# Performance work log

Hardware: AMD Instinct MI355X
Metric: run time of the kernel (lower is better)

The kernel has to match this reference:

```python
import jax, jax.numpy as jnp
import numpy as np
from jax import lax

L, B, S, D, H = 4, 4, 2048, 1024, 2048
EPS = 1e-5


def setup_inputs() -> dict:
    key = jax.random.key(0)
    ks = jax.random.split(key, 8)

    def rn(k, shape, fan_in, fan_out):
        scale = (2.0 / (fan_in + fan_out)) ** 0.5  # xavier-ish
        return jax.random.normal(k, shape, jnp.float32) * scale

    return {
        "x": jax.random.normal(ks[0], (B, S, D), jnp.float32),
        "Wp1": rn(ks[1], (L, H, D), D, H),
        "bp1": jnp.zeros((L, H), jnp.float32),
        "Wp2": rn(ks[2], (L, H, D), D, H),
        "bp2": jnp.zeros((L, H), jnp.float32),
        "convW": rn(ks[3], (L, H, H, 3), 3 * H, H),  # torch Conv1d layout (O, I, K)
        "convb": jnp.zeros((L, H), jnp.float32),
        "Wz": rn(ks[4], (L, H, H), H, H),
        "bz": jnp.zeros((L, H), jnp.float32),
        "Wh": rn(ks[5], (L, H, H), H, H),
        "bh": jnp.zeros((L, H), jnp.float32),
        "Wd": rn(ks[6], (L, D, H), H, D),
        "bd": jnp.zeros((L, D), jnp.float32),
        # 4 LayerNorms per layer: [strand1_ln1, conv_ln, gru_ln, strand2_ln1]
        "ln_g": jnp.ones((L, 4, H), jnp.float32),
        "ln_b": jnp.zeros((L, 4, H), jnp.float32),
    }


def _ln(x, g, b):
    m = jnp.mean(x, axis=-1, keepdims=True)
    xc = x - m
    v = jnp.mean(xc * xc, axis=-1, keepdims=True)
    return xc * lax.rsqrt(v + EPS) * g + b


def _log_g(x):
    return jnp.where(x >= 0, jnp.log(jax.nn.relu(x) + 0.5), -jax.nn.softplus(-x))


def _min_gru(x, Wz, bz, Wh, bh):
    # x: (B, S, H); training-mode log-space parallel scan, h_0 = 0
    k = jnp.einsum('bsh,oh->bso', x, Wz) + bz
    log_z = -jax.nn.softplus(-k)
    log_coeffs = -jax.nn.softplus(k)
    log_h0 = jnp.full((x.shape[0], 1, Wz.shape[0]), jnp.log(0.5), x.dtype)  # log_g(0)
    log_tilde_h = _log_g(jnp.einsum('bsh,oh->bso', x, Wh) + bh)
    log_values = jnp.concatenate([log_h0, log_z + log_tilde_h], axis=1)  # (B,S+1,H)
    a_star = jnp.pad(jnp.cumsum(log_coeffs, axis=1), ((0, 0), (1, 0), (0, 0)))
    log_h = a_star + lax.cumlogsumexp(log_values - a_star, axis=1)
    return jnp.exp(log_h)[:, 1:]


def _conv1d(x, w, b):
    # x: (B, S, H) -> NCH conv with kernel 3, same padding
    y = lax.conv_general_dilated(
        x.transpose(0, 2, 1), w, window_strides=(1,), padding=((1, 1),),
        dimension_numbers=('NCH', 'OIH', 'NCH'))
    return (y + b[None, :, None]).transpose(0, 2, 1)


def _forward(x, Wp1, bp1, Wp2, bp2, convW, convb, Wz, bz, Wh, bh, Wd, bd, ln_g, ln_b):
    for i in range(L):
        s1 = _ln(jnp.einsum('bsd,hd->bsh', x, Wp1[i]) + bp1[i], ln_g[i, 0], ln_b[i, 0])
        s1 = _ln(_conv1d(s1, convW[i], convb[i]), ln_g[i, 1], ln_b[i, 1])
        s1 = jax.nn.silu(s1)
        s1 = _min_gru(s1, Wz[i], bz[i], Wh[i], bh[i])
        s1 = _ln(s1, ln_g[i, 2], ln_b[i, 2])
        s2 = jax.nn.silu(_ln(jnp.einsum('bsd,hd->bsh', x, Wp2[i]) + bp2[i], ln_g[i, 3], ln_b[i, 3]))
        x = jnp.einsum('bsh,dh->bsd', s1 * s2, Wd[i]) + bd[i] + x
    return x


def reference(x, Wp1, bp1, Wp2, bp2, convW, convb, Wz, bz, Wh, bh, Wd, bd, ln_g, ln_b):
    return _forward(x, Wp1, bp1, Wp2, bp2, convW, convb, Wz, bz, Wh, bh, Wd, bd, ln_g, ln_b)
```

## Files before the change

### kernel.cpp

```cpp
#include <hip/hip_runtime.h>

typedef unsigned short u16;
typedef short  s16x8 __attribute__((ext_vector_type(8)));
typedef float  f32x4 __attribute__((ext_vector_type(4)));
typedef unsigned short u16x4 __attribute__((ext_vector_type(4)));

#define LDS_AS __attribute__((address_space(3)))
#define GLB_AS __attribute__((address_space(1)))

__device__ __forceinline__ float bf2f(u16 x) {
    unsigned u = ((unsigned)x) << 16;
    return __builtin_bit_cast(float, u);
}
__device__ __forceinline__ u16 f2bf(float f) {
    unsigned u = __builtin_bit_cast(unsigned, f);
    return (u16)((u + 0x7FFFu + ((u >> 16) & 1u)) >> 16);
}
__device__ __forceinline__ void gload16(const u16* g, u16* l) {
    __builtin_amdgcn_global_load_lds((const GLB_AS unsigned int*)g,
                                     (LDS_AS unsigned int*)l, 16, 0, 0);
}

static constexpr int Lc = 4, Sc = 2048, Dc = 1024, Hc = 2048, Mc = 8192;
static constexpr int CH = 64, CL = 32;
static constexpr int NCHAN = 4 * Hc;
static constexpr int KPW = 4096;

#define BAR() __builtin_amdgcn_s_barrier()
#define VMCNT(n) asm volatile("s_waitcnt vmcnt(" #n ")" ::: "memory")

#define READ_A(d, BUF, MH)                                                     \
    _Pragma("unroll") for (int mf = 0; mf < 4; ++mf) {                         \
        d[mf][0] = *(const s16x8*)(aB0 + (BUF)*16384 + (MH)*4096 + mf*1024);   \
        d[mf][1] = *(const s16x8*)(aB1 + (BUF)*16384 + (MH)*4096 + mf*1024);   \
    }
#define READ_B(BUF, NH)                                                        \
    _Pragma("unroll") for (int jb = 0; jb < 2; ++jb) {                         \
        bq[jb][0] = *(const s16x8*)(bB0 + (BUF)*16384 + (NH)*2048 + jb*1024);  \
        bq[jb][1] = *(const s16x8*)(bB1 + (BUF)*16384 + (NH)*2048 + jb*1024);  \
    }
#define QUAD(a, MH, NH)                                                        \
    _Pragma("unroll") for (int mf = 0; mf < 4; ++mf)                           \
    _Pragma("unroll") for (int jb = 0; jb < 2; ++jb)                           \
    _Pragma("unroll") for (int kk = 0; kk < 2; ++kk)                           \
        acc[(MH)*4 + mf][(NH)*2 + jb] = __builtin_amdgcn_mfma_f32_16x16x32_bf16( \
            a[mf][kk], bq[jb][kk], acc[(MH)*4 + mf][(NH)*2 + jb], 0, 0, 0);

#define STAGE_A(BUF, H, KT) {                                                  \
    if (CONV) {                                                                \
        const int seg_ = ((KT)*64) >> 11;                                      \
        const int kb_  = ((KT)*64) & (Hc - 1);                                 \
        const int r0_  = convRow + (H)*128 + seg_;                             \
        const u16* s0_ = ((unsigned)(r0_ - bb) < (unsigned)Sc)                 \
                             ? A + (size_t)r0_ * lda + kb_ + scol : zerobuf;   \
        const u16* s1_ = ((unsigned)(r0_ + 8 - bb) < (unsigned)Sc)             \
                             ? A + (size_t)(r0_ + 8) * lda + kb_ + scol : zerobuf; \
        gload16(s0_, ldsA + (BUF)*16384 + (H)*8192);                           \
        gload16(s1_, ldsA + (BUF)*16384 + (H)*8192 + 512);                     \
    } else {                                                                   \
        const u16* s_ = srcA + (size_t)((H)*128) * lda + (KT)*64;              \
        gload16(s_,                   ldsA + (BUF)*16384 + (H)*8192);          \
        gload16(s_ + 8*(size_t)lda,   ldsA + (BUF)*16384 + (H)*8192 + 512);    \
    } }
#define STAGE_B(BUF, H, KT) {                                                  \
    const u16* s_ = srcB + (size_t)((H)*128) * K + (KT)*64;                    \
    gload16(s_,                 ldsB + (BUF)*16384 + (H)*8192);                \
    gload16(s_ + 8*(size_t)K,   ldsB + (BUF)*16384 + (H)*8192 + 512);          \
}

template <int CONV, int REPS>
__global__ __launch_bounds__(512, 2)
void gemm8(const u16* __restrict__ A, const u16* __restrict__ Bw,
           const float* __restrict__ bias, u16* __restrict__ Cb,
           int M, int N, int K, int lda, const u16* __restrict__ zerobuf) {
    (void)M;
    __shared__ __align__(16) u16 As[2][256][64];
    __shared__ __align__(16) u16 Bs[2][256][64];

    const int tid = threadIdx.x;
    const int w = tid >> 6, l = tid & 63;
    const int wm = w & 1, wn = w >> 1;

    const unsigned nwg = gridDim.x * gridDim.y;
    unsigned id = blockIdx.x + gridDim.x * blockIdx.y;
    id = (id & 7u) * (nwg >> 3) + (id >> 3);
    const int bx = (int)(id % gridDim.x);
    const int byBase = (int)(id / gridDim.x);
    const int colBase = bx * 256;

    const int srow = w * 16 + (l >> 3);
    const int scol = ((l & 7) ^ (l >> 3)) << 3;
    const u16* srcB = Bw + (size_t)(colBase + srow) * K + scol;
    u16* const ldsA = &As[0][0][0] + w * 1024;
    u16* const ldsB = &Bs[0][0][0] + w * 1024;

    const int r16 = l & 15, slot = l >> 4;
    const int swz = (r16 & 7) << 4;
    const int co0 = (((slot << 4)      ) ^ swz) >> 1;
    const int co1 = (((slot << 4) | 64 ) ^ swz) >> 1;
    const u16* aB0 = &As[0][0][0] + (wm * 128 + r16) * 64 + co0;
    const u16* aB1 = &As[0][0][0] + (wm * 128 + r16) * 64 + co1;
    const u16* bB0 = &Bs[0][0][0] + (wn * 64  + r16) * 64 + co0;
    const u16* bB1 = &Bs[0][0][0] + (wn * 64  + r16) * 64 + co1;

    const int coll = colBase + wn * 64 + r16;

    for (int rep = 0; rep < REPS; ++rep) {
        const int rowBase = (byBase + rep * gridDim.y) * 256;
        const u16* srcA = A + (size_t)(rowBase + srow) * lda + scol;
        const int bb = rowBase & ~(Sc - 1);
        const int convRow = rowBase + srow - 1;

        f32x4 acc[8][4];
#pragma unroll
        for (int m = 0; m < 8; ++m)
#pragma unroll
            for (int n = 0; n < 4; ++n)
#pragma unroll
                for (int r = 0; r < 4; ++r) acc[m][n][r] = 0.f;

        s16x8 a0[4][2], a1[4][2], bq[2][2];

        STAGE_A(0, 0, 0); STAGE_A(0, 1, 0); STAGE_B(0, 0, 0); STAGE_B(0, 1, 0);
        VMCNT(4);
        STAGE_A(1, 0, 1); STAGE_A(1, 1, 1); STAGE_B(1, 0, 1);
        VMCNT(6);
        BAR();

        const int NI = K >> 7;
        for (int i = 0; i < NI; ++i) {
            const int t1 = 2 * i + 1, t2 = 2 * i + 2, t3 = 2 * i + 3;
            const bool more = (i + 1 < NI);
            READ_A(a0, 0, 0); READ_B(0, 0);
            STAGE_B(1, 1, t1);
            BAR();
            __builtin_amdgcn_s_setprio(1); QUAD(a0, 0, 0); __builtin_amdgcn_s_setprio(0);
            BAR();
            READ_A(a1, 0, 1);
            BAR();
            __builtin_amdgcn_s_setprio(1); QUAD(a1, 1, 0); __builtin_amdgcn_s_setprio(0);
            BAR();
            READ_B(0, 1);
            if (more) { STAGE_A(0, 0, t2); STAGE_A(0, 1, t2); }
            BAR();
            __builtin_amdgcn_s_setprio(1); QUAD(a0, 0, 1); __builtin_amdgcn_s_setprio(0);
            BAR();
            if (more) STAGE_B(0, 0, t2);
            BAR();
            __builtin_amdgcn_s_setprio(1); QUAD(a1, 1, 1); __builtin_amdgcn_s_setprio(0);
            if (more) { VMCNT(6); } else { VMCNT(0); }
            BAR();
            READ_A(a0, 1, 0); READ_B(1, 0);
            if (more) STAGE_B(0, 1, t2);
            BAR();
            __builtin_amdgcn_s_setprio(1); QUAD(a0, 0, 0); __builtin_amdgcn_s_setprio(0);
            BAR();
            READ_A(a1, 1, 1);
            BAR();
            __builtin_amdgcn_s_setprio(1); QUAD(a1, 1, 0); __builtin_amdgcn_s_setprio(0);
            BAR();
            READ_B(1, 1);
            if (more) { STAGE_A(1, 0, t3); STAGE_A(1, 1, t3); }
            BAR();
            __builtin_amdgcn_s_setprio(1); QUAD(a0, 0, 1); __builtin_amdgcn_s_setprio(0);
            BAR();
            if (more) STAGE_B(1, 0, t3);
            BAR();
            __builtin_amdgcn_s_setprio(1); QUAD(a1, 1, 1); __builtin_amdgcn_s_setprio(0);
            if (more) VMCNT(6);
            BAR();
        }

        const int row00 = rowBase + wm * 128 + slot * 4;
#pragma unroll
        for (int m8 = 0; m8 < 8; ++m8) {
#pragma unroll
            for (int n4 = 0; n4 < 4; ++n4) {
                const int col = coll + n4 * 16;
                const float bv = bias[col];
                const int row0 = row00 + m8 * 16;
#pragma unroll
                for (int r = 0; r < 4; ++r)
                    Cb[(size_t)(row0 + r) * N + col] = f2bf(acc[m8][n4][r] + bv);
            }
        }
    }
}

template <int CONV, int EPI>
__global__ __launch_bounds__(256)
void gemm_bt(const u16* __restrict__ A, const u16* __restrict__ Bw,
             const float* __restrict__ bias,
             u16* __restrict__ Cb, float* __restrict__ Cf,
             const float* __restrict__ resid, u16* __restrict__ xout,
             int M, int N, int K, int lda, const u16* __restrict__ zerobuf) {
    __shared__ __align__(16) u16 As[128 * 32];
    __shared__ __align__(16) u16 Bs[128 * 32];
    const int tid  = threadIdx.x;
    const int wave = tid >> 6, lane = tid & 63;
    const int rowBase = blockIdx.y * 128;
    const int colBase = blockIdx.x * 128;
    const int srow = tid >> 2;
    const int scol = (tid & 3) << 3;

    u16* ldsA0 = As + wave * 512;
    u16* ldsA1 = As + 2048 + wave * 512;
    u16* ldsB0 = Bs + wave * 512;
    u16* ldsB1 = Bs + 2048 + wave * 512;

    const u16* bpt0 = Bw + (size_t)(colBase + srow) * K + scol;
    const u16* bpt1 = Bw + (size_t)(colBase + 64 + srow) * K + scol;
    const int arow0 = rowBase + srow;
    const int arow1 = arow0 + 64;
    const u16* ap0 = A + (size_t)arow0 * lda + scol;
    const u16* ap1 = A + (size_t)arow1 * lda + scol;

    const int wm = wave & 1, wn = wave >> 1;
    const int mB = wm * 64, nB = wn * 64;
    const int quad = lane >> 4, l16 = lane & 15;

    f32x4 acc[4][4];
#pragma unroll
    for (int a = 0; a < 4; a++)
#pragma unroll
        for (int b = 0; b < 4; b++)
#pragma unroll
            for (int r = 0; r < 4; r++) acc[a][b][r] = 0.f;

    for (int k0 = 0; k0 < K; k0 += 32) {
        if (CONV) {
            const int seg = k0 >> 11;
            const int kk  = (k0 & (Hc - 1)) + scol;
            const int bbb = rowBase & ~(Sc - 1);
            const int r0  = arow0 + seg - 1;
            const int r1  = arow1 + seg - 1;
            const u16* g0 = ((unsigned)(r0 - bbb) < (unsigned)Sc) ? A + (size_t)r0 * lda + kk : zerobuf;
            const u16* g1 = ((unsigned)(r1 - bbb) < (unsigned)Sc) ? A + (size_t)r1 * lda + kk : zerobuf;
            gload16(g0, ldsA0);
            gload16(g1, ldsA1);
        } else {
            gload16(ap0 + k0, ldsA0);
            gload16(ap1 + k0, ldsA1);
        }
        gload16(bpt0 + k0, ldsB0);
        gload16(bpt1 + k0, ldsB1);
        __syncthreads();

        s16x8 af[4], bfr[4];
#pragma unroll
        for (int t = 0; t < 4; t++)
            af[t] = *(const s16x8*)(As + (mB + t * 16 + l16) * 32 + (quad << 3));
#pragma unroll
        for (int t = 0; t < 4; t++)
            bfr[t] = *(const s16x8*)(Bs + (nB + t * 16 + l16) * 32 + (quad << 3));
#pragma unroll
        for (int mt = 0; mt < 4; mt++)
#pragma unroll
            for (int nt = 0; nt < 4; nt++)
                acc[mt][nt] = __builtin_amdgcn_mfma_f32_16x16x32_bf16(af[mt], bfr[nt], acc[mt][nt], 0, 0, 0);
        __syncthreads();
    }

#pragma unroll
    for (int mt = 0; mt < 4; mt++) {
#pragma unroll
        for (int nt = 0; nt < 4; nt++) {
            const int col  = colBase + nB + nt * 16 + l16;
            const int row0 = rowBase + mB + mt * 16 + (quad << 2);
            const float bv = bias[col];
#pragma unroll
            for (int r = 0; r < 4; r++) {
                const size_t idx = (size_t)(row0 + r) * N + col;
                float v = acc[mt][nt][r] + bv;
                if (EPI == 0) {
                    Cb[idx] = f2bf(v);
                } else {
                    v += resid[idx];
                    Cf[idx]   = v;
                    xout[idx] = f2bf(v);
                }
            }
        }
    }
}

__global__ __launch_bounds__(256)
void ln_fuse(const u16* __restrict__ in, int instride, u16* __restrict__ out,
             const float* __restrict__ g, const float* __restrict__ b,
             const u16* __restrict__ mul, int do_silu) {
    __shared__ float sred[4], qred[4];
    const int row = blockIdx.x, tid = threadIdx.x;
    const int lane = tid & 63, wave = tid >> 6;
    const size_t ibase = (size_t)row * instride + tid * 8;
    const size_t obase = (size_t)row * Hc + tid * 8;

    s16x8 v8 = *(const s16x8*)(in + ibase);
    float x[8];
#pragma unroll
    for (int j = 0; j < 8; j++) x[j] = bf2f((u16)v8[j]);
    float s = 0.f, q = 0.f;
#pragma unroll
    for (int j = 0; j < 8; j++) { s += x[j]; q += x[j] * x[j]; }
#pragma unroll
    for (int off = 32; off > 0; off >>= 1) {
        s += __shfl_down(s, off);
        q += __shfl_down(q, off);
    }
    if (lane == 0) { sred[wave] = s; qred[wave] = q; }
    __syncthreads();
    const float St = sred[0] + sred[1] + sred[2] + sred[3];
    const float Qt = qred[0] + qred[1] + qred[2] + qred[3];
    const float mean = St * (1.0f / Hc);
    const float var  = Qt * (1.0f / Hc) - mean * mean;
    const float rs   = rsqrtf(var + 1e-5f);

    const int c = tid * 8;
    const float4 g0 = *(const float4*)(g + c), g1 = *(const float4*)(g + c + 4);
    const float4 b0 = *(const float4*)(b + c), b1 = *(const float4*)(b + c + 4);
    const float gg[8] = {g0.x, g0.y, g0.z, g0.w, g1.x, g1.y, g1.z, g1.w};
    const float bb[8] = {b0.x, b0.y, b0.z, b0.w, b1.x, b1.y, b1.z, b1.w};
    s16x8 m8;
    if (mul) m8 = *(const s16x8*)(mul + obase);
    s16x8 o8;
#pragma unroll
    for (int j = 0; j < 8; j++) {
        float y = (x[j] - mean) * rs * gg[j] + bb[j];
        if (do_silu) y = y / (1.0f + __expf(-y));
        if (mul) y *= bf2f((u16)m8[j]);
        o8[j] = (short)f2bf(y);
    }
    *(s16x8*)(out + obase) = o8;
}

__device__ __forceinline__ void scan_step(float k, float p, float& ct, float& vt) {
    const float l1p = __logf(1.f + __expf(-fabsf(k)));
    ct = -(fmaxf(k, 0.f) + l1p);
    const float lg = (p >= 0.f) ? __logf(p + 0.5f)
                                : -(fmaxf(-p, 0.f) + __logf(1.f + __expf(-fabsf(p))));
    vt = -(fmaxf(-k, 0.f) + l1p) + lg;
}
__device__ __forceinline__ float laddexp(float a, float b) {
    const float m = fmaxf(a, b);
    return m + __logf(1.f + __expf(-fabsf(a - b)));
}

__global__ __launch_bounds__(256)
void scan_part1(const u16* __restrict__ kp,
                float* __restrict__ Cc, float* __restrict__ Vv) {
    const int tid = threadIdx.x;
    const int hb = blockIdx.x & 7;
    const int c  = (blockIdx.x >> 3) & 63;
    const int b  = blockIdx.x >> 9;
    const int h  = hb * 256 + tid;
    size_t idx = (size_t)(b * Sc + c * CL) * KPW + h;
    float C = 0.f, V = -1e30f;
#pragma unroll 4
    for (int t = 0; t < CL; t++) {
        float ct, vt;
        scan_step(bf2f(kp[idx]), bf2f(kp[idx + Hc]), ct, vt);
        V = laddexp(V + ct, vt);
        C += ct;
        idx += KPW;
    }
    const int chan = b * Hc + h;
    Cc[c * NCHAN + chan] = C;
    Vv[c * NCHAN + chan] = V;
}

__global__ __launch_bounds__(256)
void scan_mid(const float* __restrict__ Cc, const float* __restrict__ Vv,
              float* __restrict__ carry) {
    const int chan = blockIdx.x * 256 + threadIdx.x;
    float lh = -0.69314718f;
    for (int cb = 0; cb < CH; cb += 8) {
        float Cr[8], Vr[8];
#pragma unroll
        for (int j = 0; j < 8; j++) {
            Cr[j] = Cc[(cb + j) * NCHAN + chan];
            Vr[j] = Vv[(cb + j) * NCHAN + chan];
        }
#pragma unroll
        for (int j = 0; j < 8; j++) {
            carry[(cb + j) * NCHAN + chan] = lh;
            lh = laddexp(lh + Cr[j], Vr[j]);
        }
    }
}

__global__ __launch_bounds__(256)
void scan_part3(const u16* __restrict__ kp,
                const float* __restrict__ carry, u16* __restrict__ out) {
    const int tid = threadIdx.x;
    const int hb = blockIdx.x & 7;
    const int c  = (blockIdx.x >> 3) & 63;
    const int b  = blockIdx.x >> 9;
    const int h  = hb * 256 + tid;
    size_t idx = (size_t)(b * Sc + c * CL) * KPW + h;
    size_t odx = (size_t)(b * Sc + c * CL) * Hc + h;
    float lh = carry[c * NCHAN + (b * Hc + h)];
#pragma unroll 4
    for (int t = 0; t < CL; t++) {
        float ct, vt;
        scan_step(bf2f(kp[idx]), bf2f(kp[idx + Hc]), ct, vt);
        lh = laddexp(lh + ct, vt);
        out[odx] = f2bf(__expf(lh));
        idx += KPW;
        odx += Hc;
    }
}

__global__ __launch_bounds__(256)
void castf2b(const float* __restrict__ in, u16* __restrict__ out, int n) {
    const int i = (blockIdx.x * 256 + threadIdx.x) << 2;
    if (i >= n) return;
    const float4 v = *(const float4*)(in + i);
    u16x4 o;
    o.x = f2bf(v.x); o.y = f2bf(v.y); o.z = f2bf(v.z); o.w = f2bf(v.w);
    *(u16x4*)(out + i) = o;
}

__global__ __launch_bounds__(256)
void prep2(const float* __restrict__ srcA, const float* __restrict__ srcB,
           const float* __restrict__ bA, const float* __restrict__ bB,
           u16* __restrict__ dst, float* __restrict__ bias_dst, int nPerHalf) {
    const int bid = blockIdx.x, tid = threadIdx.x;
    const int halfBlocks = gridDim.x >> 1;
    const int half = (bid >= halfBlocks) ? 1 : 0;
    const size_t i = ((size_t)(bid - half * halfBlocks) * 256 + tid) * 4;
    const float* src = half ? srcB : srcA;
    const float4 v = *(const float4*)(src + i);
    u16x4 o;
    o.x = f2bf(v.x); o.y = f2bf(v.y); o.z = f2bf(v.z); o.w = f2bf(v.w);
    *(u16x4*)(dst + (size_t)half * nPerHalf + i) = o;
    if (bid < 4) {
        const int j = bid * 1024 + tid * 4;
        const float4 vb = (j < 2048) ? *(const float4*)(bA + j)
                                     : *(const float4*)(bB + (j - 2048));
        *(float4*)(bias_dst + j) = vb;
    }
}

__global__ __launch_bounds__(256)
void conv_tr(const float* __restrict__ w, u16* __restrict__ out) {
    const int idx = blockIdx.x * 256 + threadIdx.x;
    const float* src = w + (size_t)idx * 3;
    const float a = src[0], b = src[1], c = src[2];
    const int o = idx >> 11, ii = idx & (Hc - 1);
    u16* dst = out + (size_t)o * (3 * Hc) + ii;
    dst[0]        = f2bf(a);
    dst[Hc]       = f2bf(b);
    dst[2 * Hc]   = f2bf(c);
}

extern "C" void kernel_launch(void* const* d_in, const int* in_sizes, int n_in,
                              void* d_out, int out_size, void* d_ws, size_t ws_size,
                              hipStream_t stream) {
    (void)in_sizes; (void)n_in; (void)out_size;
    const float* x0    = (const float*)d_in[0];
    const float* Wp1   = (const float*)d_in[1];
    const float* bp1   = (const float*)d_in[2];
    const float* Wp2   = (const float*)d_in[3];
    const float* bp2   = (const float*)d_in[4];
    const float* convW = (const float*)d_in[5];
    const float* convb = (const float*)d_in[6];
    const float* Wz    = (const float*)d_in[7];
    const float* bz    = (const float*)d_in[8];
    const float* Wh    = (const float*)d_in[9];
    const float* bh    = (const float*)d_in[10];
    const float* Wd    = (const float*)d_in[11];
    const float* bd    = (const float*)d_in[12];
    const float* lng   = (const float*)d_in[13];
    const float* lnb   = (const float*)d_in[14];
    float* out = (float*)d_out;

    char* ws = (char*)d_ws;
    u16* wbuf = (u16*)(ws);
    u16* s1   = (u16*)(ws + 25165824);
    u16* t1   = (u16*)(ws + 58720256);
    u16* kp   = (u16*)(ws + 92274688);
    u16* s2   = kp;
    u16* xb   = (u16*)(ws + 159383552);
    u16* zero = (u16*)(ws + 176160768);
    float* scanC = (float*)(ws + 176161792);
    float* scanV = (float*)(ws + 178258944);
    float* carry = (float*)(ws + 180356096);
    float* bias2 = (float*)(ws + 182453248);
    u16* P       = (u16*)(ws + 184549376);
    const bool FUSEP = ws_size >= 251658240ull;

    hipMemsetAsync(zero, 0, 1024, stream);
    castf2b<<<dim3((Mc * Dc / 4) / 256), dim3(256), 0, stream>>>(x0, xb, Mc * Dc);

    const size_t wpStride = (size_t)Hc * Dc;
    const size_t cvStride = (size_t)Hc * Hc * 3;
    const size_t wzStride = (size_t)Hc * Hc;
    const size_t wdStride = (size_t)Dc * Hc;

    for (int i = 0; i < Lc; ++i) {
        const float* g0 = lng + ((size_t)i * 4 + 0) * Hc; const float* be0 = lnb + ((size_t)i * 4 + 0) * Hc;
        const float* g1 = lng + ((size_t)i * 4 + 1) * Hc; const float* be1 = lnb + ((size_t)i * 4 + 1) * Hc;
        const float* g2 = lng + ((size_t)i * 4 + 2) * Hc; const float* be2 = lnb + ((size_t)i * 4 + 2) * Hc;
        const float* g3 = lng + ((size_t)i * 4 + 3) * Hc; const float* be3 = lnb + ((size_t)i * 4 + 3) * Hc;

        if (FUSEP) {
            prep2<<<dim3(2 * (int)(wpStride / 1024)), dim3(256), 0, stream>>>(
                Wp1 + i * wpStride, Wp2 + i * wpStride,
                bp1 + (size_t)i * Hc, bp2 + (size_t)i * Hc, wbuf, bias2, (int)wpStride);
            gemm8<0, 2><<<dim3(KPW / 256, Mc / 512), dim3(512), 0, stream>>>(
                xb, wbuf, bias2, P, Mc, KPW, Dc, Dc, zero);
            ln_fuse<<<dim3(Mc), dim3(256), 0, stream>>>(P, KPW, s1, g0, be0, nullptr, 0);
        } else {
            castf2b<<<dim3((int)(wpStride / 4 / 256)), dim3(256), 0, stream>>>(Wp1 + i * wpStride, wbuf, (int)wpStride);
            gemm8<0, 2><<<dim3(Hc / 256, Mc / 512), dim3(512), 0, stream>>>(
                xb, wbuf, bp1 + (size_t)i * Hc, t1, Mc, Hc, Dc, Dc, zero);
            ln_fuse<<<dim3(Mc), dim3(256), 0, stream>>>(t1, Hc, s1, g0, be0, nullptr, 0);
        }

        conv_tr<<<dim3((Hc * Hc) / 256), dim3(256), 0, stream>>>(convW + i * cvStride, wbuf);
        gemm8<1, 1><<<dim3(Hc / 256, Mc / 256), dim3(512), 0, stream>>>(
            s1, wbuf, convb + (size_t)i * Hc, t1, Mc, Hc, 3 * Hc, Hc, zero);
        ln_fuse<<<dim3(Mc), dim3(256), 0, stream>>>(t1, Hc, s1, g1, be1, nullptr, 1);

        prep2<<<dim3(2 * (int)(wzStride / 1024)), dim3(256), 0, stream>>>(
            Wz + i * wzStride, Wh + i * wzStride,
            bz + (size_t)i * Hc, bh + (size_t)i * Hc, wbuf, bias2, (int)wzStride);
        gemm8<0, 2><<<dim3(KPW / 256, Mc / 512), dim3(512), 0, stream>>>(
            s1, wbuf, bias2, kp, Mc, KPW, Hc, Hc, zero);
        scan_part1<<<dim3(2048), dim3(256), 0, stream>>>(kp, scanC, scanV);
        scan_mid<<<dim3(32), dim3(256), 0, stream>>>(scanC, scanV, carry);
        scan_part3<<<dim3(2048), dim3(256), 0, stream>>>(kp, carry, t1);
        ln_fuse<<<dim3(Mc), dim3(256), 0, stream>>>(t1, Hc, s1, g2, be2, nullptr, 0);

        if (FUSEP) {
            ln_fuse<<<dim3(Mc), dim3(256), 0, stream>>>(P + Hc, KPW, t1, g3, be3, s1, 1);
            castf2b<<<dim3((int)(wdStride / 4 / 256)), dim3(256), 0, stream>>>(Wd + i * wdStride, wbuf, (int)wdStride);
            gemm_bt<0, 1><<<dim3(Dc / 128, Mc / 128), dim3(256), 0, stream>>>(
                t1, wbuf, bd + (size_t)i * Dc, nullptr, out,
                (i == 0) ? x0 : out, xb, Mc, Dc, Hc, Hc, zero);
        } else {
            castf2b<<<dim3((int)(wpStride / 4 / 256)), dim3(256), 0, stream>>>(Wp2 + i * wpStride, wbuf, (int)wpStride);
            gemm8<0, 2><<<dim3(Hc / 256, Mc / 512), dim3(512), 0, stream>>>(
                xb, wbuf, bp2 + (size_t)i * Hc, t1, Mc, Hc, Dc, Dc, zero);
            ln_fuse<<<dim3(Mc), dim3(256), 0, stream>>>(t1, Hc, s2, g3, be3, s1, 1);
            castf2b<<<dim3((int)(wdStride / 4 / 256)), dim3(256), 0, stream>>>(Wd + i * wdStride, wbuf, (int)wdStride);
            gemm_bt<0, 1><<<dim3(Dc / 128, Mc / 128), dim3(256), 0, stream>>>(
                s2, wbuf, bd + (size_t)i * Dc, nullptr, out,
                (i == 0) ? x0 : out, xb, Mc, Dc, Hc, Hc, zero);
        }
    }
}
```

Baseline: 2.877 ms.

## Split GEMM A-tile staging into quarter loads and vectorize scan kernels

Restages the A tile in the main GEMM as four 64-row quarter loads per buffer. Half of them are issued one barrier phase earlier, which spreads global-to-LDS traffic more evenly across the MFMA phases. Separately, the two minGRU scan kernels now have each thread handle four adjacent channels with 8-byte vector loads and stores, cutting grid size fourfold. The risk is lower parallelism in the scan and altered vmcnt accounting in the GEMM pipeline, since the number of outstanding loads per stage changes.

```diff
diff --git a/kernel.cpp b/kernel.cpp
--- a/kernel.cpp
+++ b/kernel.cpp
@@ -46,21 +46,17 @@
         acc[(MH)*4 + mf][(NH)*2 + jb] = __builtin_amdgcn_mfma_f32_16x16x32_bf16( \
             a[mf][kk], bq[jb][kk], acc[(MH)*4 + mf][(NH)*2 + jb], 0, 0, 0);
 
-#define STAGE_A(BUF, H, KT) {                                                  \
+#define STAGE_AQ(BUF, Q, KT) {                                                 \
     if (CONV) {                                                                \
         const int seg_ = ((KT)*64) >> 11;                                      \
         const int kb_  = ((KT)*64) & (Hc - 1);                                 \
-        const int r0_  = convRow + (H)*128 + seg_;                             \
-        const u16* s0_ = ((unsigned)(r0_ - bb) < (unsigned)Sc)                 \
-                             ? A + (size_t)r0_ * lda + kb_ + scol : zerobuf;   \
-        const u16* s1_ = ((unsigned)(r0_ + 8 - bb) < (unsigned)Sc)             \
-                             ? A + (size_t)(r0_ + 8) * lda + kb_ + scol : zerobuf; \
-        gload16(s0_, ldsA + (BUF)*16384 + (H)*8192);                           \
-        gload16(s1_, ldsA + (BUF)*16384 + (H)*8192 + 512);                     \
+        const int r_   = convRowQ + (Q)*64 + seg_;                             \
+        const u16* s_ = ((unsigned)(r_ - bb) < (unsigned)Sc)                   \
+                            ? A + (size_t)r_ * lda + kb_ + scol : zerobuf;     \
+        gload16(s_, ldsAq + (BUF)*16384 + (Q)*4096);                           \
     } else {                                                                   \
-        const u16* s_ = srcA + (size_t)((H)*128) * lda + (KT)*64;              \
-        gload16(s_,                   ldsA + (BUF)*16384 + (H)*8192);          \
-        gload16(s_ + 8*(size_t)lda,   ldsA + (BUF)*16384 + (H)*8192 + 512);    \
+        gload16(srcAq + (size_t)((Q)*64) * lda + (KT)*64,                      \
+                ldsAq + (BUF)*16384 + (Q)*4096);                               \
     } }
 #define STAGE_B(BUF, H, KT) {                                                  \
     const u16* s_ = srcB + (size_t)((H)*128) * K + (KT)*64;                    \
@@ -89,10 +85,11 @@
     const int colBase = bx * 256;
 
     const int srow = w * 16 + (l >> 3);
+    const int qrow = w * 8 + (l >> 3);
     const int scol = ((l & 7) ^ (l >> 3)) << 3;
     const u16* srcB = Bw + (size_t)(colBase + srow) * K + scol;
-    u16* const ldsA = &As[0][0][0] + w * 1024;
-    u16* const ldsB = &Bs[0][0][0] + w * 1024;
+    u16* const ldsAq = &As[0][0][0] + w * 512;
+    u16* const ldsB  = &Bs[0][0][0] + w * 1024;
 
     const int r16 = l & 15, slot = l >> 4;
     const int swz = (r16 & 7) << 4;
@@ -107,9 +104,9 @@
 
     for (int rep = 0; rep < REPS; ++rep) {
         const int rowBase = (byBase + rep * gridDim.y) * 256;
-        const u16* srcA = A + (size_t)(rowBase + srow) * lda + scol;
+        const u16* srcAq = A + (size_t)(rowBase + qrow) * lda + scol;
         const int bb = rowBase & ~(Sc - 1);
-        const int convRow = rowBase + srow - 1;
+        const int convRowQ = rowBase + qrow - 1;
 
         f32x4 acc[8][4];
 #pragma unroll
@@ -121,9 +118,11 @@
 
         s16x8 a0[4][2], a1[4][2], bq[2][2];
 
-        STAGE_A(0, 0, 0); STAGE_A(0, 1, 0); STAGE_B(0, 0, 0); STAGE_B(0, 1, 0);
+        STAGE_AQ(0, 0, 0); STAGE_AQ(0, 1, 0); STAGE_AQ(0, 2, 0); STAGE_AQ(0, 3, 0);
+        STAGE_B(0, 0, 0); STAGE_B(0, 1, 0);
         VMCNT(4);
-        STAGE_A(1, 0, 1); STAGE_A(1, 1, 1); STAGE_B(1, 0, 1);
+        STAGE_AQ(1, 0, 1); STAGE_AQ(1, 1, 1); STAGE_AQ(1, 2, 1); STAGE_AQ(1, 3, 1);
+        STAGE_B(1, 0, 1);
         VMCNT(6);
         BAR();
 
@@ -137,11 +136,12 @@
             __builtin_amdgcn_s_setprio(1); QUAD(a0, 0, 0); __builtin_amdgcn_s_setprio(0);
             BAR();
             READ_A(a1, 0, 1);
+            if (more) { STAGE_AQ(0, 0, t2); STAGE_AQ(0, 2, t2); }
             BAR();
             __builtin_amdgcn_s_setprio(1); QUAD(a1, 1, 0); __builtin_amdgcn_s_setprio(0);
             BAR();
             READ_B(0, 1);
-            if (more) { STAGE_A(0, 0, t2); STAGE_A(0, 1, t2); }
+            if (more) { STAGE_AQ(0, 1, t2); STAGE_AQ(0, 3, t2); }
             BAR();
             __builtin_amdgcn_s_setprio(1); QUAD(a0, 0, 1); __builtin_amdgcn_s_setprio(0);
             BAR();
@@ -156,11 +156,12 @@
             __builtin_amdgcn_s_setprio(1); QUAD(a0, 0, 0); __builtin_amdgcn_s_setprio(0);
             BAR();
             READ_A(a1, 1, 1);
+            if (more) { STAGE_AQ(1, 0, t3); STAGE_AQ(1, 2, t3); }
             BAR();
             __builtin_amdgcn_s_setprio(1); QUAD(a1, 1, 0); __builtin_amdgcn_s_setprio(0);
             BAR();
             READ_B(1, 1);
-            if (more) { STAGE_A(1, 0, t3); STAGE_A(1, 1, t3); }
+            if (more) { STAGE_AQ(1, 1, t3); STAGE_AQ(1, 3, t3); }
             BAR();
             __builtin_amdgcn_s_setprio(1); QUAD(a0, 0, 1); __builtin_amdgcn_s_setprio(0);
             BAR();
@@ -347,24 +348,30 @@
 __global__ __launch_bounds__(256)
 void scan_part1(const u16* __restrict__ kp,
                 float* __restrict__ Cc, float* __restrict__ Vv) {
-    const int tid = threadIdx.x;
-    const int hb = blockIdx.x & 7;
-    const int c  = (blockIdx.x >> 3) & 63;
-    const int b  = blockIdx.x >> 9;
-    const int h  = hb * 256 + tid;
-    size_t idx = (size_t)(b * Sc + c * CL) * KPW + h;
-    float C = 0.f, V = -1e30f;
+    const int hb = blockIdx.x & 1;
+    const int c  = (blockIdx.x >> 1) & 63;
+    const int b  = blockIdx.x >> 7;
+    const int h0 = hb * 1024 + threadIdx.x * 4;
+    size_t base = (size_t)(b * Sc + c * CL) * KPW + h0;
+    float C[4], V[4];
+#pragma unroll
+    for (int j = 0; j < 4; j++) { C[j] = 0.f; V[j] = -1e30f; }
 #pragma unroll 4
     for (int t = 0; t < CL; t++) {
-        float ct, vt;
-        scan_step(bf2f(kp[idx]), bf2f(kp[idx + Hc]), ct, vt);
-        V = laddexp(V + ct, vt);
-        C += ct;
-        idx += KPW;
-    }
-    const int chan = b * Hc + h;
-    Cc[c * NCHAN + chan] = C;
-    Vv[c * NCHAN + chan] = V;
+        const u16x4 k4 = *(const u16x4*)(kp + base);
+        const u16x4 p4 = *(const u16x4*)(kp + base + Hc);
+#pragma unroll
+        for (int j = 0; j < 4; j++) {
+            float ct, vt;
+            scan_step(bf2f(k4[j]), bf2f(p4[j]), ct, vt);
+            V[j] = laddexp(V[j] + ct, vt);
+            C[j] += ct;
+        }
+        base += KPW;
+    }
+    const int chan0 = b * Hc + h0;
+    *(float4*)(Cc + c * NCHAN + chan0) = *(const float4*)C;
+    *(float4*)(Vv + c * NCHAN + chan0) = *(const float4*)V;
 }
 
 __global__ __launch_bounds__(256)
@@ -390,22 +397,29 @@
 __global__ __launch_bounds__(256)
 void scan_part3(const u16* __restrict__ kp,
                 const float* __restrict__ carry, u16* __restrict__ out) {
-    const int tid = threadIdx.x;
-    const int hb = blockIdx.x & 7;
-    const int c  = (blockIdx.x >> 3) & 63;
-    const int b  = blockIdx.x >> 9;
-    const int h  = hb * 256 + tid;
-    size_t idx = (size_t)(b * Sc + c * CL) * KPW + h;
-    size_t odx = (size_t)(b * Sc + c * CL) * Hc + h;
-    float lh = carry[c * NCHAN + (b * Hc + h)];
+    const int hb = blockIdx.x & 1;
+    const int c  = (blockIdx.x >> 1) & 63;
+    const int b  = blockIdx.x >> 7;
+    const int h0 = hb * 1024 + threadIdx.x * 4;
+    size_t base = (size_t)(b * Sc + c * CL) * KPW + h0;
+    size_t obase = (size_t)(b * Sc + c * CL) * Hc + h0;
+    const float4 cr = *(const float4*)(carry + c * NCHAN + (b * Hc + h0));
+    float lh[4] = {cr.x, cr.y, cr.z, cr.w};
 #pragma unroll 4
     for (int t = 0; t < CL; t++) {
-        float ct, vt;
-        scan_step(bf2f(kp[idx]), bf2f(kp[idx + Hc]), ct, vt);
-        lh = laddexp(lh + ct, vt);
-        out[odx] = f2bf(__expf(lh));
-        idx += KPW;
-        odx += Hc;
+        const u16x4 k4 = *(const u16x4*)(kp + base);
+        const u16x4 p4 = *(const u16x4*)(kp + base + Hc);
+        u16x4 o4;
+#pragma unroll
+        for (int j = 0; j < 4; j++) {
+            float ct, vt;
+            scan_step(bf2f(k4[j]), bf2f(p4[j]), ct, vt);
+            lh[j] = laddexp(lh[j] + ct, vt);
+            o4[j] = f2bf(__expf(lh[j]));
+        }
+        *(u16x4*)(out + obase) = o4;
+        base += KPW;
+        obase += Hc;
     }
 }
 
@@ -526,9 +540,9 @@
             bz + (size_t)i * Hc, bh + (size_t)i * Hc, wbuf, bias2, (int)wzStride);
         gemm8<0, 2><<<dim3(KPW / 256, Mc / 512), dim3(512), 0, stream>>>(
             s1, wbuf, bias2, kp, Mc, KPW, Hc, Hc, zero);
-        scan_part1<<<dim3(2048), dim3(256), 0, stream>>>(kp, scanC, scanV);
+        scan_part1<<<dim3(512), dim3(256), 0, stream>>>(kp, scanC, scanV);
         scan_mid<<<dim3(32), dim3(256), 0, stream>>>(scanC, scanV, carry);
-        scan_part3<<<dim3(2048), dim3(256), 0, stream>>>(kp, carry, t1);
+        scan_part3<<<dim3(512), dim3(256), 0, stream>>>(kp, carry, t1);
         ln_fuse<<<dim3(Mc), dim3(256), 0, stream>>>(t1, Hc, s1, g2, be2, nullptr, 0);
 
         if (FUSEP) {
```

Result: slower. 3.157 ms (+9.7%).
